# Kernel optimization log

Hardware: AMD Instinct MI355X
Metric: run time of the kernel (lower is better)

The kernel has to match this reference:

```python
import jax, jax.numpy as jnp
import numpy as np

HEADS = 8
DIM_HEAD = 64
IMG = 32            # image_size
K = 5               # kernel_size
DIL = 1             # dilation
SEQ_LEN = 1279
SCALE = DIM_HEAD ** -0.5
IMG_SEQ = IMG * IMG                 # 1024
TEXT_LEN = SEQ_LEN + 1 - IMG_SEQ    # 256
NEG = -np.finfo(np.float32).max


def _unfold(img, pad_value):
    """torch F.unfold equivalent. img: [B, C, H, W] -> [B, H*W, K*K, C].
    Kernel-position index j is fastest-varying (matches torch unfold ordering
    after rearrange 'b (d j) i -> b i j d')."""
    B, C, H, W = img.shape
    p = ((K - 1) * DIL + 1) // 2
    padded = jnp.pad(img, ((0, 0), (0, 0), (p, p), (p, p)), constant_values=pad_value)
    patches = [padded[:, :, i * DIL:i * DIL + H, j * DIL:j * DIL + W]
               for i in range(K) for j in range(K)]
    pt = jnp.stack(patches, axis=2)            # [B, C, K*K, H, W]
    return pt.reshape(B, C, K * K, H * W).transpose(0, 3, 2, 1)


def _split_heads(t, b):
    # [b, N, h*d] -> [(b h), N, d]  (b slow, h fast)
    N = t.shape[1]
    return t.reshape(b, N, HEADS, DIM_HEAD).transpose(0, 2, 1, 3).reshape(b * HEADS, N, DIM_HEAD)


def setup_inputs() -> dict:
    key = jax.random.key(0)
    k1, k2, k3, k4 = jax.random.split(key, 4)
    dim = 512
    inner = HEADS * DIM_HEAD
    x = jax.random.normal(k1, (4, 1279, dim), dtype=jnp.float32)
    mask = jnp.ones((4, TEXT_LEN), dtype=bool)
    W_qkv = jax.random.normal(k2, (dim, inner * 3), dtype=jnp.float32) * 0.02
    W_out = jax.random.normal(k3, (inner, dim), dtype=jnp.float32) * 0.02
    b_out = jax.random.normal(k4, (dim,), dtype=jnp.float32) * 0.02
    return {"x": x, "mask": mask, "W_qkv": W_qkv, "W_out": W_out, "b_out": b_out}


def reference(x, mask, W_qkv, W_out, b_out):
    b, n, dim = x.shape
    pad = SEQ_LEN - n + 1
    xp = jnp.pad(x, ((0, 0), (0, pad), (0, 0)))            # [b, SEQ_LEN+1, dim]
    mask = mask[:, :TEXT_LEN]

    qkv = xp @ W_qkv
    q, k, v = jnp.split(qkv, 3, axis=-1)
    q = _split_heads(q, b) * SCALE                          # [(bh), N, d]
    k = _split_heads(k, b)
    v = _split_heads(v, b)

    q_text, q_img = q[:, :-IMG_SEQ], q[:, -IMG_SEQ:]
    k_text, k_img = k[:, :-IMG_SEQ], k[:, -IMG_SEQ:]
    v_text, v_img = v[:, :-IMG_SEQ], v[:, -IMG_SEQ:]

    # ---- text-to-text causal attention ----
    dots_text = jnp.einsum('bid,bjd->bij', q_text, k_text)
    tl = TEXT_LEN
    text_causal = jnp.triu(jnp.ones((tl, tl), dtype=bool), 1)
    dots_text = jnp.where(text_causal[None], NEG, dots_text)
    attn_text = jax.nn.softmax(dots_text, axis=-1)
    out_text = jnp.einsum('bij,bjd->bid', attn_text, v_text)

    # ---- local-window image attention (unfold) ----
    bh = b * HEADS
    k_img2 = k_img.reshape(bh, IMG, IMG, DIM_HEAD).transpose(0, 3, 1, 2)
    v_img2 = v_img.reshape(bh, IMG, IMG, DIM_HEAD).transpose(0, 3, 1, 2)
    k_imgu = _unfold(k_img2, 0.0)                           # [(bh), IMG_SEQ, K*K, d]
    v_imgu = _unfold(v_img2, 0.0)

    dots_image = jnp.einsum('bid,bijd->bij', q_img, k_imgu)         # [(bh), IMG_SEQ, K*K]
    dots_i2t = jnp.einsum('bid,bjd->bij', q_img, k_text)            # [(bh), IMG_SEQ, tl]

    # causal mask over local window via unfolded position indices
    idx = jnp.arange(IMG_SEQ, dtype=jnp.float32).reshape(1, 1, IMG, IMG)
    k_idx = _unfold(idx, float(IMG_SEQ))[..., 0]            # [1, IMG_SEQ, K*K]
    q_idx = jnp.arange(IMG_SEQ, dtype=jnp.float32)[None, :, None]
    causal_mask = q_idx < k_idx                             # [1, IMG_SEQ, K*K]

    text_pad_mask = jnp.repeat(~mask, HEADS, axis=0)[:, None, :]    # [(bh), 1, tl]
    full_mask = jnp.concatenate([
        jnp.broadcast_to(text_pad_mask, (bh, IMG_SEQ, tl)),
        jnp.broadcast_to(causal_mask, (bh, IMG_SEQ, K * K)),
    ], axis=-1)

    dots = jnp.concatenate([dots_i2t, dots_image], axis=-1)
    dots = jnp.where(full_mask, NEG, dots)
    attn = jax.nn.softmax(dots, axis=-1)
    attn_i2t, attn_img = attn[..., :tl], attn[..., tl:]

    out_image = (jnp.einsum('bij,bijd->bid', attn_img, v_imgu)
                 + jnp.einsum('bij,bjd->bid', attn_i2t, v_text))

    # ---- merge and project ----
    out = jnp.concatenate([out_text, out_image], axis=1)    # [(bh), N, d]
    N = out.shape[1]
    out = out.reshape(b, HEADS, N, DIM_HEAD).transpose(0, 2, 1, 3).reshape(b, N, HEADS * DIM_HEAD)
    out = out @ W_out + b_out
    return out[:, :n]
```

## Files before the change

kernel.cpp:

```cpp
#include <hip/hip_runtime.h>
#include <hip/hip_bf16.h>
#include <math.h>

#define HEADS   8
#define DH      64
#define IMGW    32
#define KKER    5
#define SEQ     1280
#define NTOK    1279
#define TL      256
#define IMG_SEQ 1024
#define DIM     512
#define BATCH   4
#define BH      32
#define SCALE   0.125f
#define NEGB    (-1.0e30f)

#define WQN  (DIM * 3 * DIM)
#define WON  (DIM * DIM)
#define QKVN ((size_t)BH * SEQ * DH)
#define AON  ((size_t)BATCH * SEQ * DIM)

#define XPBLK   1280
#define WQTILES 768
#define WOTILES 256


typedef unsigned short u16;
typedef __attribute__((ext_vector_type(8))) short bf16x8;
typedef __attribute__((ext_vector_type(4))) float f32x4;

__device__ inline u16 f2b(float f) {
    unsigned int u = __float_as_uint(f);
    return (u16)((u + 0x7FFFu + ((u >> 16) & 1u)) >> 16);
}
__device__ inline unsigned pack2(float a, float b) {
    return (unsigned)f2b(a) | ((unsigned)f2b(b) << 16);
}

__device__ inline void ldsload16(const u16* g, u16* l) {
    __builtin_amdgcn_global_load_lds(
        (const __attribute__((address_space(1))) unsigned int*)g,
        (__attribute__((address_space(3))) unsigned int*)l, 16, 0, 0);
}

__device__ inline void lds_barrier() {
    asm volatile("s_waitcnt lgkmcnt(0)\n\ts_barrier" ::: "memory");
}

__global__ __launch_bounds__(256) void cvt_all(
    const float* __restrict__ x, const float* __restrict__ Wq,
    const float* __restrict__ Wo, u16* __restrict__ xbf,
    u16* __restrict__ WqT, u16* __restrict__ WoT)
{
    __shared__ u16 tile[32][33];
    const int b = blockIdx.x;
    if (b < XPBLK) {
        const int i = b * 256 + threadIdx.x;
        const int row = i >> 6;
        const int bb = row / SEQ, nn = row % SEQ;
        union { unsigned u[4]; bf16x8 v; } r;
        if (nn < NTOK) {
            const size_t j = ((size_t)(bb * NTOK + nn) * 128 + (i & 63) * 2);
            const float4 a = ((const float4*)x)[j];
            const float4 c = ((const float4*)x)[j + 1];
            r.u[0] = pack2(a.x, a.y); r.u[1] = pack2(a.z, a.w);
            r.u[2] = pack2(c.x, c.y); r.u[3] = pack2(c.z, c.w);
        } else {
            r.u[0] = r.u[1] = r.u[2] = r.u[3] = 0u;
        }
        ((bf16x8*)xbf)[i] = r.v;
        return;
    }
    int t = b - XPBLK;
    const float* src; u16* dst; int C;
    if (t < WQTILES) { src = Wq; dst = WqT; C = 3 * DIM; }
    else             { t -= WQTILES; src = Wo; dst = WoT; C = DIM; }
    const int tc = C / 32;
    const int tr0 = (t / tc) * 32, tc0 = (t % tc) * 32;
    const int ty = threadIdx.x >> 5, tx = threadIdx.x & 31;
    #pragma unroll
    for (int s = 0; s < 4; s++) {
        const int r = ty + 8 * s;
        tile[r][tx] = f2b(src[(size_t)(tr0 + r) * C + tc0 + tx]);
    }
    __syncthreads();
    #pragma unroll
    for (int s = 0; s < 4; s++) {
        const int c = ty + 8 * s;
        dst[(size_t)(tc0 + c) * DIM + tr0 + tx] = tile[tx][c];
    }
}

__global__ __launch_bounds__(256) void qkv_mfma6(
    const u16* __restrict__ xbf, const u16* __restrict__ WqT,
    u16* __restrict__ Qbf, u16* __restrict__ Ktl, u16* __restrict__ Vtl)
{
    __shared__ u16 pool[12288];
    u16* const buf0 = pool;
    u16* const buf1 = pool + 6144;
    const int tid  = threadIdx.x;
    const int lane = tid & 63, wave = tid >> 6;
    const int quad = lane >> 4, l16 = lane & 15;
    const int wm = (wave >> 1) * 32, wn = (wave & 1) * 64;

    const int id  = blockIdx.x;
    const int nid = (id & 7) * 120 + (id >> 3);
    const int m0 = (nid / 12) * 64, n0 = (nid % 12) * 128;

    const u16* ga  = xbf + (size_t)(m0 + (tid >> 2)) * DIM + (tid & 3) * 8;
    const u16* gb0 = WqT + (size_t)(n0 + (tid >> 2)) * DIM + (tid & 3) * 8;
    const u16* gb1 = WqT + (size_t)(n0 + 64 + (tid >> 2)) * DIM + (tid & 3) * 8;

    f32x4 acc[2][4];
    #pragma unroll
    for (int i = 0; i < 2; i++)
        #pragma unroll
        for (int j = 0; j < 4; j++) acc[i][j] = (f32x4){0.f, 0.f, 0.f, 0.f};

    auto stage = [&](u16* b, int k) {
        ldsload16(ga  + k, b + wave * 512);
        ldsload16(gb0 + k, b + 2048 + wave * 512);
        ldsload16(gb1 + k, b + 4096 + wave * 512);
    };
    auto comp = [&](const u16* b) {
        bf16x8 af_[2], bf_[4];
        #pragma unroll
        for (int i = 0; i < 2; i++)
            af_[i] = *(const bf16x8*)&b[(wm + i * 16 + l16) * 32 + quad * 8];
        #pragma unroll
        for (int j = 0; j < 4; j++)
            bf_[j] = *(const bf16x8*)&b[2048 + (wn + j * 16 + l16) * 32 + quad * 8];
        #pragma unroll
        for (int i = 0; i < 2; i++)
            #pragma unroll
            for (int j = 0; j < 4; j++)
                acc[i][j] = __builtin_amdgcn_mfma_f32_16x16x32_bf16(
                    af_[i], bf_[j], acc[i][j], 0, 0, 0);
    };

    stage(buf0, 0);
    stage(buf1, 32);
    #pragma unroll
    for (int s = 0; s < 16; s++) {
        if (s == 15) asm volatile("s_waitcnt vmcnt(0)" ::: "memory");
        else         asm volatile("s_waitcnt vmcnt(3)" ::: "memory");
        __builtin_amdgcn_s_barrier();
        comp((s & 1) ? buf1 : buf0);
        asm volatile("s_waitcnt lgkmcnt(0)" ::: "memory");
        __builtin_amdgcn_sched_barrier(0);
        __builtin_amdgcn_s_barrier();
        if (s < 14) stage((s & 1) ? buf1 : buf0, 32 * (s + 2));
    }

    const int which = n0 >> 9;
    const float scl = (which == 0) ? SCALE : 1.f;
    __syncthreads();
    #pragma unroll
    for (int i = 0; i < 2; i++)
        #pragma unroll
        for (int r = 0; r < 4; r++)
            #pragma unroll
            for (int j = 0; j < 4; j++)
                pool[(wm + i * 16 + quad * 4 + r) * 144 + wn + j * 16 + l16] =
                    f2b(acc[i][j][r] * scl);
    __syncthreads();

    const int b_  = m0 / SEQ;
    const int nn0 = m0 % SEQ;
    if (which == 0) {
        #pragma unroll
        for (int s = 0; s < 4; s++) {
            const int c   = tid + 256 * s;
            const int row = c >> 4, c8 = (c & 15) * 8;
            const int col511 = (n0 + c8) & 511;
            const int h = col511 >> 6, d0 = col511 & 63;
            const int bhh = b_ * HEADS + h;
            const bf16x8 v = *(const bf16x8*)&pool[row * 144 + c8];
            *(bf16x8*)&Qbf[((size_t)bhh * SEQ + nn0 + row) * DH + d0] = v;
        }
    } else if (which == 1) {
        #pragma unroll
        for (int s = 0; s < 4; s++) {
            const int c   = tid + 256 * s;
            const int row = c >> 4, c8 = (c & 15) * 8;
            const int col511 = (n0 + c8) & 511;
            const int h = col511 >> 6, d0 = col511 & 63;
            const int bhh = b_ * HEADS + h;
            const int key = nn0 + row;
            const bf16x8 v = *(const bf16x8*)&pool[row * 144 + c8];
            *(bf16x8*)&Ktl[(size_t)bhh * 81920 +
                (size_t)((((key >> 4) * 2 + (d0 >> 5)) * 512) +
                         ((key & 15) + 16 * ((d0 >> 3) & 3)) * 8)] = v;
        }
    } else {
        #pragma unroll
        for (int s = 0; s < 4; s++) {
            const int c   = tid + 256 * s;
            const int col = c & 127, r8 = (c >> 7) * 8;
            const int col511 = (n0 + col) & 511;
            const int h = col511 >> 6, d = col511 & 63;
            const int bhh = b_ * HEADS + h;
            const int key0 = nn0 + r8;
            union { u16 u[8]; bf16x8 v; } w;
            #pragma unroll
            for (int k = 0; k < 8; k++)
                w.u[k] = pool[(r8 + k) * 144 + col];
            *(bf16x8*)&Vtl[(size_t)bhh * 81920 +
                (size_t)((((key0 >> 5) * 4 + (d >> 4)) * 512) +
                         ((d & 15) + 16 * ((r8 >> 3) & 3)) * 8)] = w.v;
        }
    }
}

__global__ __launch_bounds__(256, 4) void attn_fused(
    const u16* __restrict__ Qbf, const u16* __restrict__ Ktl,
    const u16* __restrict__ Vtl, u16* __restrict__ AObf)
{
    const int id = blockIdx.x;
    const int bh = (id & 7) | (((id >> 3) & 3) << 3);
    const int bx = id >> 5;
    const bool istext = bx < 8;
    const int r0 = bx - 8;
    const int qt0 = istext ? bx * 32 : r0 * 32;
    const int qrow0 = istext ? qt0 : TL + qt0;
    const int tid = threadIdx.x;
    const int lane = tid & 63, wave = tid >> 6;
    const int quad = lane >> 4, l16 = lane & 15;

    __shared__ float Opool[4][2176];
    __shared__ float msm[4][32];
    __shared__ float mss[4][32];

    const int krs = istext ? 0 : min(max(r0 - 2, 0), IMGW - 5);
    const int cbase = TL + krs * 32;
    const bool tactive = !istext || (2 * wave <= bx);
    const bool xtra = (!istext) && (wave == 0);

    u16* const Pw = (u16*)Opool[wave];

    bf16x8 af[2][2];
    #pragma unroll
    for (int i = 0; i < 2; i++) {
        const u16* qr = Qbf + ((size_t)bh * SEQ + qrow0 + i * 16 + l16) * DH;
        af[i][0] = *(const bf16x8*)(qr + quad * 8);
        af[i][1] = *(const bf16x8*)(qr + 32 + quad * 8);
    }

    const u16* kt = Ktl + (size_t)bh * 81920;

    f32x4 sacc[2][4], cacc[2][2], xacc[2][2];
    #pragma unroll
    for (int i = 0; i < 2; i++) {
        #pragma unroll
        for (int j = 0; j < 4; j++) sacc[i][j] = (f32x4){0.f, 0.f, 0.f, 0.f};
        #pragma unroll
        for (int s = 0; s < 2; s++) {
            cacc[i][s] = (f32x4){0.f, 0.f, 0.f, 0.f};
            xacc[i][s] = (f32x4){0.f, 0.f, 0.f, 0.f};
        }
    }

    if (tactive) {
        bf16x8 kf0[4], kf1[4];
        #pragma unroll
        for (int j = 0; j < 4; j++) {
            kf0[j] = *(const bf16x8*)&kt[(size_t)(((wave * 4 + j) * 2) * 512) + lane * 8];
            kf1[j] = *(const bf16x8*)&kt[(size_t)(((wave * 4 + j) * 2 + 1) * 512) + lane * 8];
        }
        #pragma unroll
        for (int j = 0; j < 4; j++)
            #pragma unroll
            for (int i = 0; i < 2; i++) {
                sacc[i][j] = __builtin_amdgcn_mfma_f32_16x16x32_bf16(af[i][0], kf0[j], sacc[i][j], 0, 0, 0);
                sacc[i][j] = __builtin_amdgcn_mfma_f32_16x16x32_bf16(af[i][1], kf1[j], sacc[i][j], 0, 0, 0);
            }
    }
    if (!istext) {
        const int cb16 = cbase >> 4;
        {
            bf16x8 cf0[2], cf1[2];
            #pragma unroll
            for (int s = 0; s < 2; s++) {
                const int blk = cb16 + 2 * wave + s;
                cf0[s] = *(const bf16x8*)&kt[(size_t)((blk * 2) * 512) + lane * 8];
                cf1[s] = *(const bf16x8*)&kt[(size_t)((blk * 2 + 1) * 512) + lane * 8];
            }
            #pragma unroll
            for (int s = 0; s < 2; s++)
                #pragma unroll
                for (int i = 0; i < 2; i++) {
                    cacc[i][s] = __builtin_amdgcn_mfma_f32_16x16x32_bf16(af[i][0], cf0[s], cacc[i][s], 0, 0, 0);
                    cacc[i][s] = __builtin_amdgcn_mfma_f32_16x16x32_bf16(af[i][1], cf1[s], cacc[i][s], 0, 0, 0);
                }
        }
        if (xtra) {
            bf16x8 cf0[2], cf1[2];
            #pragma unroll
            for (int s = 0; s < 2; s++) {
                const int blk = cb16 + 8 + s;
                cf0[s] = *(const bf16x8*)&kt[(size_t)((blk * 2) * 512) + lane * 8];
                cf1[s] = *(const bf16x8*)&kt[(size_t)((blk * 2 + 1) * 512) + lane * 8];
            }
            #pragma unroll
            for (int s = 0; s < 2; s++)
                #pragma unroll
                for (int i = 0; i < 2; i++) {
                    xacc[i][s] = __builtin_amdgcn_mfma_f32_16x16x32_bf16(af[i][0], cf0[s], xacc[i][s], 0, 0, 0);
                    xacc[i][s] = __builtin_amdgcn_mfma_f32_16x16x32_bf16(af[i][1], cf1[s], xacc[i][s], 0, 0, 0);
                }
        }
    }

    float m8[2][4];
    #pragma unroll
    for (int i = 0; i < 2; i++)
        #pragma unroll
        for (int r = 0; r < 4; r++) {
            const int q = i * 16 + quad * 4 + r;
            float m = NEGB;
            if (istext) {
                if (tactive) {
                    const int qg = qt0 + q;
                    #pragma unroll
                    for (int j = 0; j < 4; j++) {
                        const int key = wave * 64 + j * 16 + l16;
                        const float v = (key <= qg) ? sacc[i][j][r] : NEGB;
                        sacc[i][j][r] = v;
                        m = fmaxf(m, v);
                    }
                }
            } else {
                const int qi = qt0 + q;
                #pragma unroll
                for (int j = 0; j < 4; j++) m = fmaxf(m, sacc[i][j][r]);
                #pragma unroll
                for (int s = 0; s < 2; s++) {
                    const int t = 2 * wave + s;
                    const int kidx = krs * 32 + t * 16 + l16;
                    const int kr = kidx >> 5, kc = kidx & 31;
                    const bool valid = (abs(kr - r0) <= 2) && (abs(kc - q) <= 2)
                                       && (kidx <= qi);
                    const float v = valid ? cacc[i][s][r] : NEGB;
                    cacc[i][s][r] = v;
                    m = fmaxf(m, v);
                }
                if (xtra) {
                    #pragma unroll
                    for (int s = 0; s < 2; s++) {
                        const int t = 8 + s;
                        const int kidx = krs * 32 + t * 16 + l16;
                        const int kr = kidx >> 5, kc = kidx & 31;
                        const bool valid = (abs(kr - r0) <= 2) && (abs(kc - q) <= 2)
                                           && (kidx <= qi);
                        const float v = valid ? xacc[i][s][r] : NEGB;
                        xacc[i][s][r] = v;
                        m = fmaxf(m, v);
                    }
                }
            }
            m8[i][r] = m;
        }
    #pragma unroll
    for (int off = 1; off < 16; off <<= 1)
        #pragma unroll
        for (int i = 0; i < 2; i++)
            #pragma unroll
            for (int r = 0; r < 4; r++)
                m8[i][r] = fmaxf(m8[i][r], __shfl_xor(m8[i][r], off));

    float s8[2][4];
    #pragma unroll
    for (int i = 0; i < 2; i++)
        #pragma unroll
        for (int r = 0; r < 4; r++) {
            const int q = i * 16 + quad * 4 + r;
            const float mr = m8[i][r];
            float s = 0.f;
            if (tactive) {
                #pragma unroll
                for (int j = 0; j < 4; j++) {
                    const float p = __expf(sacc[i][j][r] - mr);
                    Pw[q * 136 + j * 16 + l16] = f2b(p);
                    s += p;
                }
            }
            if (!istext) {
                #pragma unroll
                for (int ss = 0; ss < 2; ss++) {
                    const float p = __expf(cacc[i][ss][r] - mr);
                    Pw[q * 136 + 64 + ss * 16 + l16] = f2b(p);
                    s += p;
                }
                if (xtra) {
                    #pragma unroll
                    for (int ss = 0; ss < 2; ss++) {
                        const float p = __expf(xacc[i][ss][r] - mr);
                        Pw[q * 136 + 96 + ss * 16 + l16] = f2b(p);
                        s += p;
                    }
                }
            }
            s8[i][r] = s;
        }
    #pragma unroll
    for (int off = 1; off < 16; off <<= 1)
        #pragma unroll
        for (int i = 0; i < 2; i++)
            #pragma unroll
            for (int r = 0; r < 4; r++)
                s8[i][r] += __shfl_xor(s8[i][r], off);
    if (l16 == 0)
        #pragma unroll
        for (int i = 0; i < 2; i++)
            #pragma unroll
            for (int r = 0; r < 4; r++) {
                const int q = i * 16 + quad * 4 + r;
                msm[wave][q] = m8[i][r];
                mss[wave][q] = s8[i][r];
            }
    asm volatile("s_waitcnt lgkmcnt(0)" ::: "memory");

    bool cact[4];
    int ck[4];
    ck[0] = wave * 64; ck[1] = wave * 64 + 32;
    ck[2] = cbase + wave * 32; ck[3] = cbase + 128;
    if (istext) {
        cact[0] = tactive; cact[1] = (2 * wave + 1 <= bx);
        cact[2] = false;   cact[3] = false;
    } else {
        cact[0] = cact[1] = cact[2] = true; cact[3] = (wave == 0);
    }

    const u16* vt = Vtl + (size_t)bh * 81920;
    f32x4 o2[2][4];
    #pragma unroll
    for (int i = 0; i < 2; i++)
        #pragma unroll
        for (int j = 0; j < 4; j++) o2[i][j] = (f32x4){0.f, 0.f, 0.f, 0.f};

    #pragma unroll
    for (int c = 0; c < 4; c++) {
        if (cact[c]) {
            const bf16x8 av0 = *(const bf16x8*)&Pw[l16 * 136 + c * 32 + quad * 8];
            const bf16x8 av1 = *(const bf16x8*)&Pw[(16 + l16) * 136 + c * 32 + quad * 8];
            const int kcb = (ck[c] >> 5) * 4;
            bf16x8 bv[4];
            #pragma unroll
            for (int j = 0; j < 4; j++)
                bv[j] = *(const bf16x8*)&vt[(size_t)((kcb + j) * 512) + lane * 8];
            #pragma unroll
            for (int j = 0; j < 4; j++) {
                o2[0][j] = __builtin_amdgcn_mfma_f32_16x16x32_bf16(av0, bv[j], o2[0][j], 0, 0, 0);
                o2[1][j] = __builtin_amdgcn_mfma_f32_16x16x32_bf16(av1, bv[j], o2[1][j], 0, 0, 0);
            }
        }
    }

    #pragma unroll
    for (int i = 0; i < 2; i++)
        #pragma unroll
        for (int j = 0; j < 4; j++)
            #pragma unroll
            for (int r = 0; r < 4; r++)
                Opool[wave][(i * 16 + quad * 4 + r) * 68 + j * 16 + l16] = o2[i][j][r];

    lds_barrier();

    const int qq = tid >> 3, d8 = (tid & 7) * 8;
    const float mm = fmaxf(fmaxf(msm[0][qq], msm[1][qq]),
                           fmaxf(msm[2][qq], msm[3][qq]));
    float wgt[4];
    float den = 0.f;
    #pragma unroll
    for (int w = 0; w < 4; w++) {
        wgt[w] = __expf(msm[w][qq] - mm);
        den += mss[w][qq] * wgt[w];
    }
    float o[8];
    #pragma unroll
    for (int e = 0; e < 8; e++) o[e] = 0.f;
    #pragma unroll
    for (int w = 0; w < 4; w++) {
        const float* Ow = &Opool[w][qq * 68 + d8];
        #pragma unroll
        for (int e = 0; e < 8; e++) o[e] += Ow[e] * wgt[w];
    }
    const float inv = 1.f / den;
    union { u16 u[8]; bf16x8 v; } pk;
    #pragma unroll
    for (int e = 0; e < 8; e++) pk.u[e] = f2b(o[e] * inv);
    const int b_ = bh >> 3, h = bh & 7;
    *(bf16x8*)&AObf[((size_t)b_ * SEQ + qrow0 + qq) * DIM + h * DH + d8] = pk.v;
}

__global__ __launch_bounds__(256) void proj_mfma6(
    const u16* __restrict__ AObf, const u16* __restrict__ WoT,
    const float* __restrict__ bias, float* __restrict__ out)
{
    __shared__ u16 pool[10240];
    u16* const buf0 = pool;
    u16* const buf1 = pool + 5120;
    const int tid  = threadIdx.x;
    const int lane = tid & 63, wave = tid >> 6;
    const int quad = lane >> 4, l16 = lane & 15;
    const int wm = (wave >> 1) * 16, wn = (wave & 1) * 64;

    const int id  = blockIdx.x;
    const int nid = (id & 7) * 80 + (id >> 3);
    const int m0 = (nid / 4) * 32, n0 = (nid % 4) * 128;

    const u16* ga  = AObf + (size_t)(m0 + ((tid & 127) >> 2)) * DIM + (tid & 3) * 8;
    const u16* gb0 = WoT + (size_t)(n0 + (tid >> 2)) * DIM + (tid & 3) * 8;
    const u16* gb1 = WoT + (size_t)(n0 + 64 + (tid >> 2)) * DIM + (tid & 3) * 8;

    f32x4 acc[4];
    #pragma unroll
    for (int j = 0; j < 4; j++) acc[j] = (f32x4){0.f, 0.f, 0.f, 0.f};

    auto stage = [&](u16* b, int k) {
        if (wave < 2) ldsload16(ga + k, b + (wave & 1) * 512);
        ldsload16(gb0 + k, b + 1024 + wave * 512);
        ldsload16(gb1 + k, b + 3072 + wave * 512);
    };
    auto comp = [&](const u16* b) {
        const bf16x8 af = *(const bf16x8*)&b[(wm + l16) * 32 + quad * 8];
        bf16x8 bf_[4];
        #pragma unroll
        for (int j = 0; j < 4; j++)
            bf_[j] = *(const bf16x8*)&b[1024 + (wn + j * 16 + l16) * 32 + quad * 8];
        #pragma unroll
        for (int j = 0; j < 4; j++)
            acc[j] = __builtin_amdgcn_mfma_f32_16x16x32_bf16(af, bf_[j], acc[j], 0, 0, 0);
    };

    stage(buf0, 0);
    stage(buf1, 32);
    #pragma unroll
    for (int s = 0; s < 16; s++) {
        if (s == 15)        asm volatile("s_waitcnt vmcnt(0)" ::: "memory");
        else if (wave < 2)  asm volatile("s_waitcnt vmcnt(3)" ::: "memory");
        else                asm volatile("s_waitcnt vmcnt(2)" ::: "memory");
        __builtin_amdgcn_s_barrier();
        comp((s & 1) ? buf1 : buf0);
        asm volatile("s_waitcnt lgkmcnt(0)" ::: "memory");
        __builtin_amdgcn_sched_barrier(0);
        __builtin_amdgcn_s_barrier();
        if (s < 14) stage((s & 1) ? buf1 : buf0, 32 * (s + 2));
    }

    #pragma unroll
    for (int r = 0; r < 4; r++) {
        const int mm = m0 + wm + quad * 4 + r;
        const int bb = mm / SEQ, nn = mm % SEQ;
        if (nn >= NTOK) continue;
        const size_t mr = (size_t)(bb * NTOK + nn);
        #pragma unroll
        for (int j = 0; j < 4; j++) {
            const int ncol = n0 + wn + j * 16 + l16;
            out[mr * DIM + ncol] = acc[j][r] + bias[ncol];
        }
    }
}

extern "C" void kernel_launch(void* const* d_in, const int* in_sizes, int n_in,
                              void* d_out, int out_size, void* d_ws, size_t ws_size,
                              hipStream_t stream)
{
    const float* x    = (const float*)d_in[0];
    const float* Wqkv = (const float*)d_in[2];
    const float* Wout = (const float*)d_in[3];
    const float* bout = (const float*)d_in[4];
    float* out = (float*)d_out;

    u16* wsu  = (u16*)d_ws;
    u16* xbf  = wsu;
    u16* WqT  = xbf + AON;
    u16* WoT  = WqT + WQN;
    u16* Qbf  = WoT + WON;
    u16* Ktl  = Qbf + QKVN;
    u16* Vtl  = Ktl + QKVN;
    u16* AObf = Vtl + QKVN;

    cvt_all   <<<XPBLK + WQTILES + WOTILES, 256, 0, stream>>>(x, Wqkv, Wout, xbf, WqT, WoT);
    qkv_mfma6 <<<dim3(960), 256, 0, stream>>>(xbf, WqT, Qbf, Ktl, Vtl);
    attn_fused<<<dim3(40 * BH), 256, 0, stream>>>(Qbf, Ktl, Vtl, AObf);
    proj_mfma6<<<dim3(640), 256, 0, stream>>>(AObf, WoT, bout, out);
}
```

Before: 116.6 us.

## Halve attention query tile to 16 rows, use exp2 softmax, drop barrier

The fused attention kernel now gives each block 16 query rows instead of 32, doubling the grid to 80×BH blocks. The launch-bounds hint rises to 6 blocks per SIMD, and registers and LDS shrink to match. The goal is more parallelism and occupancy, at the cost of each block reloading the same K/V fragments for half as many queries. Log2(e) is folded into the Q scale in the QKV kernel so the softmax can use exp2f. A __syncthreads before the epilogue LDS writes in the QKV kernel is also removed, relying on the barrier that ends the compute loop.

```diff
diff --git a/kernel.cpp b/kernel.cpp
--- a/kernel.cpp
+++ b/kernel.cpp
@@ -14,6 +14,7 @@
 #define BATCH   4
 #define BH      32
 #define SCALE   0.125f
+#define QSCALE  (0.125f * 1.44269504088896f)
 #define NEGB    (-1.0e30f)
 
 #define WQN  (DIM * 3 * DIM)
@@ -28,6 +29,7 @@
 
 typedef unsigned short u16;
 typedef __attribute__((ext_vector_type(8))) short bf16x8;
+typedef __attribute__((ext_vector_type(4))) short bf16x4;
 typedef __attribute__((ext_vector_type(4))) float f32x4;
 
 __device__ inline u16 f2b(float f) {
@@ -154,8 +156,7 @@
     }
 
     const int which = n0 >> 9;
-    const float scl = (which == 0) ? SCALE : 1.f;
-    __syncthreads();
+    const float scl = (which == 0) ? QSCALE : 1.f;
     #pragma unroll
     for (int i = 0; i < 2; i++)
         #pragma unroll
@@ -213,52 +214,46 @@
     }
 }
 
-__global__ __launch_bounds__(256, 4) void attn_fused(
+__global__ __launch_bounds__(256, 6) void attn_fused(
     const u16* __restrict__ Qbf, const u16* __restrict__ Ktl,
     const u16* __restrict__ Vtl, u16* __restrict__ AObf)
 {
     const int id = blockIdx.x;
     const int bh = (id & 7) | (((id >> 3) & 3) << 3);
     const int bx = id >> 5;
-    const bool istext = bx < 8;
-    const int r0 = bx - 8;
-    const int qt0 = istext ? bx * 32 : r0 * 32;
+    const bool istext = bx < 16;
+    const int it = bx - 16;
+    const int r0 = it >> 1;
+    const int qt0 = istext ? bx * 16 : it * 16;
     const int qrow0 = istext ? qt0 : TL + qt0;
     const int tid = threadIdx.x;
     const int lane = tid & 63, wave = tid >> 6;
     const int quad = lane >> 4, l16 = lane & 15;
 
-    __shared__ float Opool[4][2176];
-    __shared__ float msm[4][32];
-    __shared__ float mss[4][32];
+    __shared__ float Opool[4][1088];
+    __shared__ float msm[4][16];
+    __shared__ float mss[4][16];
 
     const int krs = istext ? 0 : min(max(r0 - 2, 0), IMGW - 5);
     const int cbase = TL + krs * 32;
-    const bool tactive = !istext || (2 * wave <= bx);
+    const bool tactive = !istext || (4 * wave <= bx);
     const bool xtra = (!istext) && (wave == 0);
 
     u16* const Pw = (u16*)Opool[wave];
 
-    bf16x8 af[2][2];
-    #pragma unroll
-    for (int i = 0; i < 2; i++) {
-        const u16* qr = Qbf + ((size_t)bh * SEQ + qrow0 + i * 16 + l16) * DH;
-        af[i][0] = *(const bf16x8*)(qr + quad * 8);
-        af[i][1] = *(const bf16x8*)(qr + 32 + quad * 8);
-    }
+    const u16* qr = Qbf + ((size_t)bh * SEQ + qrow0 + l16) * DH;
+    const bf16x8 af0 = *(const bf16x8*)(qr + quad * 8);
+    const bf16x8 af1 = *(const bf16x8*)(qr + 32 + quad * 8);
 
     const u16* kt = Ktl + (size_t)bh * 81920;
 
-    f32x4 sacc[2][4], cacc[2][2], xacc[2][2];
-    #pragma unroll
-    for (int i = 0; i < 2; i++) {
-        #pragma unroll
-        for (int j = 0; j < 4; j++) sacc[i][j] = (f32x4){0.f, 0.f, 0.f, 0.f};
-        #pragma unroll
-        for (int s = 0; s < 2; s++) {
-            cacc[i][s] = (f32x4){0.f, 0.f, 0.f, 0.f};
-            xacc[i][s] = (f32x4){0.f, 0.f, 0.f, 0.f};
-        }
+    f32x4 sacc[4], cacc[2], xacc[2];
+    #pragma unroll
+    for (int j = 0; j < 4; j++) sacc[j] = (f32x4){0.f, 0.f, 0.f, 0.f};
+    #pragma unroll
+    for (int s = 0; s < 2; s++) {
+        cacc[s] = (f32x4){0.f, 0.f, 0.f, 0.f};
+        xacc[s] = (f32x4){0.f, 0.f, 0.f, 0.f};
     }
 
     if (tactive) {
@@ -269,12 +264,10 @@
             kf1[j] = *(const bf16x8*)&kt[(size_t)(((wave * 4 + j) * 2 + 1) * 512) + lane * 8];
         }
         #pragma unroll
-        for (int j = 0; j < 4; j++)
-            #pragma unroll
-            for (int i = 0; i < 2; i++) {
-                sacc[i][j] = __builtin_amdgcn_mfma_f32_16x16x32_bf16(af[i][0], kf0[j], sacc[i][j], 0, 0, 0);
-                sacc[i][j] = __builtin_amdgcn_mfma_f32_16x16x32_bf16(af[i][1], kf1[j], sacc[i][j], 0, 0, 0);
-            }
+        for (int j = 0; j < 4; j++) {
+            sacc[j] = __builtin_amdgcn_mfma_f32_16x16x32_bf16(af0, kf0[j], sacc[j], 0, 0, 0);
+            sacc[j] = __builtin_amdgcn_mfma_f32_16x16x32_bf16(af1, kf1[j], sacc[j], 0, 0, 0);
+        }
     }
     if (!istext) {
         const int cb16 = cbase >> 4;
@@ -287,12 +280,10 @@
                 cf1[s] = *(const bf16x8*)&kt[(size_t)((blk * 2 + 1) * 512) + lane * 8];
             }
             #pragma unroll
-            for (int s = 0; s < 2; s++)
-                #pragma unroll
-                for (int i = 0; i < 2; i++) {
-                    cacc[i][s] = __builtin_amdgcn_mfma_f32_16x16x32_bf16(af[i][0], cf0[s], cacc[i][s], 0, 0, 0);
-                    cacc[i][s] = __builtin_amdgcn_mfma_f32_16x16x32_bf16(af[i][1], cf1[s], cacc[i][s], 0, 0, 0);
-                }
+            for (int s = 0; s < 2; s++) {
+                cacc[s] = __builtin_amdgcn_mfma_f32_16x16x32_bf16(af0, cf0[s], cacc[s], 0, 0, 0);
+                cacc[s] = __builtin_amdgcn_mfma_f32_16x16x32_bf16(af1, cf1[s], cacc[s], 0, 0, 0);
+            }
         }
         if (xtra) {
             bf16x8 cf0[2], cf1[2];
@@ -303,122 +294,109 @@
                 cf1[s] = *(const bf16x8*)&kt[(size_t)((blk * 2 + 1) * 512) + lane * 8];
             }
             #pragma unroll
-            for (int s = 0; s < 2; s++)
+            for (int s = 0; s < 2; s++) {
+                xacc[s] = __builtin_amdgcn_mfma_f32_16x16x32_bf16(af0, cf0[s], xacc[s], 0, 0, 0);
+                xacc[s] = __builtin_amdgcn_mfma_f32_16x16x32_bf16(af1, cf1[s], xacc[s], 0, 0, 0);
+            }
+        }
+    }
+
+    float m4[4];
+    #pragma unroll
+    for (int r = 0; r < 4; r++) {
+        const int q = quad * 4 + r;
+        float m = NEGB;
+        if (istext) {
+            if (tactive) {
+                const int qg = qt0 + q;
                 #pragma unroll
-                for (int i = 0; i < 2; i++) {
-                    xacc[i][s] = __builtin_amdgcn_mfma_f32_16x16x32_bf16(af[i][0], cf0[s], xacc[i][s], 0, 0, 0);
-                    xacc[i][s] = __builtin_amdgcn_mfma_f32_16x16x32_bf16(af[i][1], cf1[s], xacc[i][s], 0, 0, 0);
+                for (int j = 0; j < 4; j++) {
+                    const int key = wave * 64 + j * 16 + l16;
+                    const float v = (key <= qg) ? sacc[j][r] : NEGB;
+                    sacc[j][r] = v;
+                    m = fmaxf(m, v);
                 }
-        }
-    }
-
-    float m8[2][4];
-    #pragma unroll
-    for (int i = 0; i < 2; i++)
-        #pragma unroll
-        for (int r = 0; r < 4; r++) {
-            const int q = i * 16 + quad * 4 + r;
-            float m = NEGB;
-            if (istext) {
-                if (tactive) {
-                    const int qg = qt0 + q;
-                    #pragma unroll
-                    for (int j = 0; j < 4; j++) {
-                        const int key = wave * 64 + j * 16 + l16;
-                        const float v = (key <= qg) ? sacc[i][j][r] : NEGB;
-                        sacc[i][j][r] = v;
-                        m = fmaxf(m, v);
-                    }
-                }
-            } else {
-                const int qi = qt0 + q;
-                #pragma unroll
-                for (int j = 0; j < 4; j++) m = fmaxf(m, sacc[i][j][r]);
+            }
+        } else {
+            const int qi = qt0 + q;
+            #pragma unroll
+            for (int j = 0; j < 4; j++) m = fmaxf(m, sacc[j][r]);
+            #pragma unroll
+            for (int s = 0; s < 2; s++) {
+                const int t = 2 * wave + s;
+                const int kidx = krs * 32 + t * 16 + l16;
+                const int kr = kidx >> 5, kc = kidx & 31;
+                const bool valid = (abs(kr - r0) <= 2) && (abs(kc - qi % 32) <= 2)
+                                   && (kidx <= qi);
+                const float v = valid ? cacc[s][r] : NEGB;
+                cacc[s][r] = v;
+                m = fmaxf(m, v);
+            }
+            if (xtra) {
                 #pragma unroll
                 for (int s = 0; s < 2; s++) {
-                    const int t = 2 * wave + s;
+                    const int t = 8 + s;
                     const int kidx = krs * 32 + t * 16 + l16;
                     const int kr = kidx >> 5, kc = kidx & 31;
-                    const bool valid = (abs(kr - r0) <= 2) && (abs(kc - q) <= 2)
+                    const bool valid = (abs(kr - r0) <= 2) && (abs(kc - qi % 32) <= 2)
                                        && (kidx <= qi);
-                    const float v = valid ? cacc[i][s][r] : NEGB;
-                    cacc[i][s][r] = v;
+                    const float v = valid ? xacc[s][r] : NEGB;
+                    xacc[s][r] = v;
                     m = fmaxf(m, v);
                 }
-                if (xtra) {
-                    #pragma unroll
-                    for (int s = 0; s < 2; s++) {
-                        const int t = 8 + s;
-                        const int kidx = krs * 32 + t * 16 + l16;
-                        const int kr = kidx >> 5, kc = kidx & 31;
-                        const bool valid = (abs(kr - r0) <= 2) && (abs(kc - q) <= 2)
-                                           && (kidx <= qi);
-                        const float v = valid ? xacc[i][s][r] : NEGB;
-                        xacc[i][s][r] = v;
-                        m = fmaxf(m, v);
-                    }
-                }
-            }
-            m8[i][r] = m;
-        }
+            }
+        }
+        m4[r] = m;
+    }
     #pragma unroll
     for (int off = 1; off < 16; off <<= 1)
         #pragma unroll
-        for (int i = 0; i < 2; i++)
-            #pragma unroll
-            for (int r = 0; r < 4; r++)
-                m8[i][r] = fmaxf(m8[i][r], __shfl_xor(m8[i][r], off));
-
-    float s8[2][4];
-    #pragma unroll
-    for (int i = 0; i < 2; i++)
-        #pragma unroll
-        for (int r = 0; r < 4; r++) {
-            const int q = i * 16 + quad * 4 + r;
-            const float mr = m8[i][r];
-            float s = 0.f;
-            if (tactive) {
+        for (int r = 0; r < 4; r++)
+            m4[r] = fmaxf(m4[r], __shfl_xor(m4[r], off));
+
+    float s4[4];
+    #pragma unroll
+    for (int r = 0; r < 4; r++) {
+        const int q = quad * 4 + r;
+        const float mr = m4[r];
+        float s = 0.f;
+        if (tactive) {
+            #pragma unroll
+            for (int j = 0; j < 4; j++) {
+                const float p = exp2f(sacc[j][r] - mr);
+                Pw[q * 136 + j * 16 + l16] = f2b(p);
+                s += p;
+            }
+        }
+        if (!istext) {
+            #pragma unroll
+            for (int ss = 0; ss < 2; ss++) {
+                const float p = exp2f(cacc[ss][r] - mr);
+                Pw[q * 136 + 64 + ss * 16 + l16] = f2b(p);
+                s += p;
+            }
+            if (xtra) {
                 #pragma unroll
-                for (int j = 0; j < 4; j++) {
-                    const float p = __expf(sacc[i][j][r] - mr);
-                    Pw[q * 136 + j * 16 + l16] = f2b(p);
+                for (int ss = 0; ss < 2; ss++) {
+                    const float p = exp2f(xacc[ss][r] - mr);
+                    Pw[q * 136 + 96 + ss * 16 + l16] = f2b(p);
                     s += p;
                 }
             }
-            if (!istext) {
-                #pragma unroll
-                for (int ss = 0; ss < 2; ss++) {
-                    const float p = __expf(cacc[i][ss][r] - mr);
-                    Pw[q * 136 + 64 + ss * 16 + l16] = f2b(p);
-                    s += p;
-                }
-                if (xtra) {
-                    #pragma unroll
-                    for (int ss = 0; ss < 2; ss++) {
-                        const float p = __expf(xacc[i][ss][r] - mr);
-                        Pw[q * 136 + 96 + ss * 16 + l16] = f2b(p);
-                        s += p;
-                    }
-                }
-            }
-            s8[i][r] = s;
-        }
+        }
+        s4[r] = s;
+    }
     #pragma unroll
     for (int off = 1; off < 16; off <<= 1)
         #pragma unroll
-        for (int i = 0; i < 2; i++)
-            #pragma unroll
-            for (int r = 0; r < 4; r++)
-                s8[i][r] += __shfl_xor(s8[i][r], off);
+        for (int r = 0; r < 4; r++)
+            s4[r] += __shfl_xor(s4[r], off);
     if (l16 == 0)
         #pragma unroll
-        for (int i = 0; i < 2; i++)
-            #pragma unroll
-            for (int r = 0; r < 4; r++) {
-                const int q = i * 16 + quad * 4 + r;
-                msm[wave][q] = m8[i][r];
-                mss[wave][q] = s8[i][r];
-            }
+        for (int r = 0; r < 4; r++) {
+            msm[wave][quad * 4 + r] = m4[r];
+            mss[wave][quad * 4 + r] = s4[r];
+        }
     asm volatile("s_waitcnt lgkmcnt(0)" ::: "memory");
 
     bool cact[4];
@@ -426,72 +404,66 @@
     ck[0] = wave * 64; ck[1] = wave * 64 + 32;
     ck[2] = cbase + wave * 32; ck[3] = cbase + 128;
     if (istext) {
-        cact[0] = tactive; cact[1] = (2 * wave + 1 <= bx);
-        cact[2] = false;   cact[3] = false;
+        cact[0] = tactive;
+        cact[1] = (bx >= 4 * wave + 2);
+        cact[2] = false; cact[3] = false;
     } else {
         cact[0] = cact[1] = cact[2] = true; cact[3] = (wave == 0);
     }
 
     const u16* vt = Vtl + (size_t)bh * 81920;
-    f32x4 o2[2][4];
-    #pragma unroll
-    for (int i = 0; i < 2; i++)
-        #pragma unroll
-        for (int j = 0; j < 4; j++) o2[i][j] = (f32x4){0.f, 0.f, 0.f, 0.f};
+    f32x4 o2[4];
+    #pragma unroll
+    for (int j = 0; j < 4; j++) o2[j] = (f32x4){0.f, 0.f, 0.f, 0.f};
 
     #pragma unroll
     for (int c = 0; c < 4; c++) {
         if (cact[c]) {
-            const bf16x8 av0 = *(const bf16x8*)&Pw[l16 * 136 + c * 32 + quad * 8];
-            const bf16x8 av1 = *(const bf16x8*)&Pw[(16 + l16) * 136 + c * 32 + quad * 8];
+            const bf16x8 av = *(const bf16x8*)&Pw[l16 * 136 + c * 32 + quad * 8];
             const int kcb = (ck[c] >> 5) * 4;
             bf16x8 bv[4];
             #pragma unroll
             for (int j = 0; j < 4; j++)
                 bv[j] = *(const bf16x8*)&vt[(size_t)((kcb + j) * 512) + lane * 8];
             #pragma unroll
-            for (int j = 0; j < 4; j++) {
-                o2[0][j] = __builtin_amdgcn_mfma_f32_16x16x32_bf16(av0, bv[j], o2[0][j], 0, 0, 0);
-                o2[1][j] = __builtin_amdgcn_mfma_f32_16x16x32_bf16(av1, bv[j], o2[1][j], 0, 0, 0);
-            }
-        }
-    }
-
-    #pragma unroll
-    for (int i = 0; i < 2; i++)
-        #pragma unroll
-        for (int j = 0; j < 4; j++)
-            #pragma unroll
-            for (int r = 0; r < 4; r++)
-                Opool[wave][(i * 16 + quad * 4 + r) * 68 + j * 16 + l16] = o2[i][j][r];
+            for (int j = 0; j < 4; j++)
+                o2[j] = __builtin_amdgcn_mfma_f32_16x16x32_bf16(av, bv[j], o2[j], 0, 0, 0);
+        }
+    }
+
+    #pragma unroll
+    for (int j = 0; j < 4; j++)
+        #pragma unroll
+        for (int r = 0; r < 4; r++)
+            Opool[wave][(quad * 4 + r) * 68 + j * 16 + l16] = o2[j][r];
 
     lds_barrier();
 
-    const int qq = tid >> 3, d8 = (tid & 7) * 8;
+    const int qq = tid >> 4, d4 = (tid & 15) * 4;
     const float mm = fmaxf(fmaxf(msm[0][qq], msm[1][qq]),
                            fmaxf(msm[2][qq], msm[3][qq]));
     float wgt[4];
     float den = 0.f;
     #pragma unroll
     for (int w = 0; w < 4; w++) {
-        wgt[w] = __expf(msm[w][qq] - mm);
+        wgt[w] = exp2f(msm[w][qq] - mm);
         den += mss[w][qq] * wgt[w];
     }
-    float o[8];
-    #pragma unroll
-    for (int e = 0; e < 8; e++) o[e] = 0.f;
+    float o[4];
+    #pragma unroll
+    for (int e = 0; e < 4; e++) o[e] = 0.f;
     #pragma unroll
     for (int w = 0; w < 4; w++) {
-        const float* Ow = &Opool[w][qq * 68 + d8];
-        #pragma unroll
-        for (int e = 0; e < 8; e++) o[e] += Ow[e] * wgt[w];
+        const float* Ow = &Opool[w][qq * 68 + d4];
+        #pragma unroll
+        for (int e = 0; e < 4; e++) o[e] += Ow[e] * wgt[w];
     }
     const float inv = 1.f / den;
-    union { u16 u[8]; bf16x8 v; } pk;
-    #pragma unroll
-    for (int e = 0; e < 8; e++) pk.u[e] = f2b(o[e] * inv);
+    union { u16 u[4]; bf16x4 v; } pk;
+    #pragma unroll
+    for (int e = 0; e < 4; e++) pk.u[e] = f2b(o[e] * inv);
     const int b_ = bh >> 3, h = bh & 7;
-    *(bf16x8*)&AObf[((size_t)b_ * SEQ + qrow0 + qq) * DIM + h * DH + d8] = pk.v;
+    *(bf16x4*)&AObf[((size_t)b_ * SEQ + qrow0 + qq) * DIM + h * DH + d4] = pk.v;
 }
 
 __global__ __launch_bounds__(256) void proj_mfma6(
@@ -584,6 +556,6 @@
 
     cvt_all   <<<XPBLK + WQTILES + WOTILES, 256, 0, stream>>>(x, Wqkv, Wout, xbf, WqT, WoT);
     qkv_mfma6 <<<dim3(960), 256, 0, stream>>>(xbf, WqT, Qbf, Ktl, Vtl);
-    attn_fused<<<dim3(40 * BH), 256, 0, stream>>>(Qbf, Ktl, Vtl, AObf);
+    attn_fused<<<dim3(80 * BH), 256, 0, stream>>>(Qbf, Ktl, Vtl, AObf);
     proj_mfma6<<<dim3(640), 256, 0, stream>>>(AObf, WoT, bout, out);
 }
```

After: 115.2 us. No clear change (-1.1%).
